# Kernel optimization log

Measured on AMD Instinct MI355X. Metric: run time of the kernel, lower is better.

## Reference

```python
import jax, jax.numpy as jnp
import numpy as np

B, R, A, K, O, I = 50000, 5, 8, 2, 32, 32


def setup_inputs() -> dict:
    key = jax.random.key(0)
    k1, k2, k3 = jax.random.split(key, 3)
    signal = jax.random.normal(k1, (B, R, A, 3, I), dtype=jnp.float32)
    bary = jax.random.uniform(k2, (B, R, A, 3), dtype=jnp.float32)
    # glorot-uniform-ish kernel: shape (R, A, K, O, I)
    limit = np.sqrt(6.0 / (I + O)).astype(np.float32)
    kernel = jax.random.uniform(k3, (R, A, K, O, I), dtype=jnp.float32,
                                minval=-limit, maxval=limit)
    return {"signal": signal, "bary": bary, "kernel": kernel}


def reference(signal, bary, kernel):
    # Barycentric interpolation: pullback[b,r,a,i] = sum_t bary[b,r,a,t] * signal[b,r,a,t,i]
    pullback = jnp.einsum('brat,brati->brai', bary, signal)  # (B,R,A,I)

    n_rot = kernel.shape[1]  # A rotations
    # rotated angular indices: rot_idx[c, a] = (a + c) % A
    rot_idx = (jnp.arange(n_rot)[:, None] + jnp.arange(n_rot)[None, :]) % n_rot
    k_rot = kernel[:, rot_idx]  # (R, C=A, A, K, O, I)

    # conv[b,c,o] = sum_{r,a,k,i} kernel[r,(a+c)%A,k,o,i] * pullback[b,r,a,i]
    conv = jnp.einsum('brai,rcakoi->bco', pullback, k_rot)  # (B, C, O)
    act = jax.nn.relu(conv)

    # Angular max pooling: pick rotation with max euclidean norm over O
    norms = jnp.linalg.norm(act, axis=-1)          # (B, C)
    best = jnp.argmax(norms, axis=-1)              # (B,)
    out = jnp.take_along_axis(act, best[:, None, None], axis=1)[:, 0]  # (B, O)
    return out
```

## Files before the change

kernel.cpp:

```cpp
#include <hip/hip_runtime.h>


#define B_TOT 50000
#define NRA 40

typedef __attribute__((ext_vector_type(8))) short short8v;
typedef __attribute__((ext_vector_type(4))) float f32x4;

__device__ __align__(16) unsigned short W_hi_g[NRA * 256 * 32];
__device__ __align__(16) unsigned short W_lo_g[NRA * 256 * 32];

static __device__ __forceinline__ unsigned short f2bf(float x) {
    unsigned u = __float_as_uint(x);
    u += 0x7FFFu + ((u >> 16) & 1u);
    return (unsigned short)(u >> 16);
}
static __device__ __forceinline__ float bf2f(unsigned short h) {
    return __uint_as_float(((unsigned)h) << 16);
}

static __device__ __forceinline__ void lds_barrier() {
    asm volatile("s_waitcnt lgkmcnt(0)" ::: "memory");
    __builtin_amdgcn_s_barrier();
    asm volatile("" ::: "memory");
}

__global__ __launch_bounds__(256) void build_w_kernel(const float* __restrict__ kern) {
    int e = blockIdx.x * 256 + threadIdx.x;
    int i = e & 31;
    int n = (e >> 5) & 255;
    int ra = e >> 13;
    int r = ra >> 3, a = ra & 7;
    int c = n >> 5, o = n & 31;
    int a2 = (c + a) & 7;
    const float* p = kern + ((((r * 8 + a2) * 2) * 32 + o) * 32 + i);
    float w = p[0] + p[1024];
    unsigned short hi = f2bf(w);
    unsigned short lo = f2bf(w - bf2f(hi));
    W_hi_g[e] = hi;
    W_lo_g[e] = lo;
}

static __device__ __forceinline__ void pcomp(float by0, float by1, float by2,
                                             const float4& a, const float4& b,
                                             const float4& c, float* d) {
    d[0] = fmaf(by2, c.x, fmaf(by1, b.x, by0 * a.x));
    d[1] = fmaf(by2, c.y, fmaf(by1, b.y, by0 * a.y));
    d[2] = fmaf(by2, c.z, fmaf(by1, b.z, by0 * a.z));
    d[3] = fmaf(by2, c.w, fmaf(by1, b.w, by0 * a.w));
}

static __device__ __forceinline__ void pack_write(unsigned short* buf, int idx, const float* v) {
    unsigned short h[4], l[4];
#pragma unroll
    for (int k = 0; k < 4; ++k) {
        h[k] = f2bf(v[k]);
        l[k] = f2bf(v[k] - bf2f(h[k]));
    }
    uint2 H, L;
    H.x = (unsigned)h[0] | ((unsigned)h[1] << 16);
    H.y = (unsigned)h[2] | ((unsigned)h[3] << 16);
    L.x = (unsigned)l[0] | ((unsigned)l[1] << 16);
    L.y = (unsigned)l[2] | ((unsigned)l[3] << 16);
    *(uint2*)(buf + idx) = H;
    *(uint2*)(buf + 2560 + idx) = L;
}

__global__ __launch_bounds__(256, 3) void conv_geo_kernel(const float* __restrict__ sig,
                                                          const float* __restrict__ bary,
                                                          float* __restrict__ out) {
    __shared__ __align__(16) float smem[8448];
    unsigned short* pb0 = (unsigned short*)smem;
    unsigned short* pb1 = pb0 + 5120;

    const int tid  = threadIdx.x;
    const int lane = tid & 63;
    const int wave = tid >> 6;
    const int b_l  = tid >> 2;
    const int q    = tid & 3;
    const int b0   = blockIdx.x * 64;
    int bld = b0 + b_l; if (bld > B_TOT - 1) bld = B_TOT - 1;
    const size_t sig_row = (size_t)bld * 40;

    f32x4 acc[4][4];
#pragma unroll
    for (int mi = 0; mi < 4; ++mi)
#pragma unroll
        for (int ni = 0; ni < 4; ++ni) acc[mi][ni] = (f32x4){0.f, 0.f, 0.f, 0.f};

    const int wcol = (wave * 64 + (lane & 15)) * 32 + (lane >> 4) * 8;
    const int poff = (lane & 15) * 40 + (lane >> 4) * 8;
    const int widx = b_l * 40 + q * 4;

    float4 s0, s1, s2, s3, s4, s5;
    float by0, by1, by2;
    auto load_sig = [&](int ra) {
        const float* sp = sig + (sig_row + ra) * 96 + q * 4;
        s0 = *(const float4*)(sp);      s1 = *(const float4*)(sp + 16);
        s2 = *(const float4*)(sp + 32); s3 = *(const float4*)(sp + 48);
        s4 = *(const float4*)(sp + 64); s5 = *(const float4*)(sp + 80);
        const float* bp = bary + (sig_row + ra) * 3;
        by0 = bp[0]; by1 = bp[1]; by2 = bp[2];
    };
    auto store_p = [&](unsigned short* wrbuf) {
        float pa[4], pbv[4];
        pcomp(by0, by1, by2, s0, s2, s4, pa);
        pcomp(by0, by1, by2, s1, s3, s5, pbv);
        pack_write(wrbuf, widx, pa);
        pack_write(wrbuf, widx + 16, pbv);
    };

    load_sig(0);
    store_p(pb0);
    load_sig(1);
    lds_barrier();

    auto body = [&](int ra, unsigned short* rdbuf, unsigned short* wrbuf) {
        if (ra + 1 < NRA) store_p(wrbuf);
        short8v bh[4], bl[4];
        const unsigned short* whp = W_hi_g + ra * 8192 + wcol;
        const unsigned short* wlp = W_lo_g + ra * 8192 + wcol;
#pragma unroll
        for (int ni = 0; ni < 4; ++ni) {
            bh[ni] = *(const short8v*)(whp + ni * 512);
            bl[ni] = *(const short8v*)(wlp + ni * 512);
        }
        if (ra + 2 < NRA) load_sig(ra + 2);
#pragma unroll
        for (int mi = 0; mi < 4; ++mi) {
            const unsigned short* pr = rdbuf + mi * 640 + poff;
            short8v ah = *(const short8v*)pr;
            short8v al = *(const short8v*)(pr + 2560);
#pragma unroll
            for (int ni = 0; ni < 4; ++ni) {
                acc[mi][ni] = __builtin_amdgcn_mfma_f32_16x16x32_bf16(ah, bh[ni], acc[mi][ni], 0, 0, 0);
                acc[mi][ni] = __builtin_amdgcn_mfma_f32_16x16x32_bf16(ah, bl[ni], acc[mi][ni], 0, 0, 0);
                acc[mi][ni] = __builtin_amdgcn_mfma_f32_16x16x32_bf16(al, bh[ni], acc[mi][ni], 0, 0, 0);
            }
        }
        lds_barrier();
    };

    for (int ra = 0; ra < NRA; ra += 2) {
        body(ra,     pb0, pb1);
        body(ra + 1, pb1, pb0);
    }

    const int colb = wave * 64 + (lane & 15);
    const int rsub = (lane >> 4) * 4;
#pragma unroll
    for (int ph = 0; ph < 2; ++ph) {
        __syncthreads();
#pragma unroll
        for (int mh = 0; mh < 2; ++mh) {
            int mi = ph * 2 + mh;
#pragma unroll
            for (int ni = 0; ni < 4; ++ni)
#pragma unroll
                for (int j = 0; j < 4; ++j)
                    smem[(mh * 16 + rsub + j) * 264 + colb + ni * 16] =
                        fmaxf(acc[mi][ni][j], 0.0f);
        }
        __syncthreads();
        int bb = tid >> 3;
        int c  = tid & 7;
        float n2 = 0.0f;
#pragma unroll
        for (int t = 0; t < 8; ++t) {
            float4 v = *(const float4*)&smem[bb * 264 + c * 32 + t * 4];
            n2 = fmaf(v.x, v.x, n2); n2 = fmaf(v.y, v.y, n2);
            n2 = fmaf(v.z, v.z, n2); n2 = fmaf(v.w, v.w, n2);
        }
        int bc = c;
#pragma unroll
        for (int m = 1; m < 8; m <<= 1) {
            float on2 = __shfl_xor(n2, m, 64);
            int obc = __shfl_xor(bc, m, 64);
            if (on2 > n2 || (on2 == n2 && obc < bc)) { n2 = on2; bc = obc; }
        }
        int b = b0 + ph * 32 + bb;
        if (b < B_TOT) {
            float4 v = *(const float4*)&smem[bb * 264 + bc * 32 + (tid & 7) * 4];
            *(float4*)&out[(size_t)b * 32 + (tid & 7) * 4] = v;
        }
    }
}

extern "C" void kernel_launch(void* const* d_in, const int* in_sizes, int n_in,
                              void* d_out, int out_size, void* d_ws, size_t ws_size,
                              hipStream_t stream) {
    const float* sig  = (const float*)d_in[0];
    const float* bary = (const float*)d_in[1];
    const float* kern = (const float*)d_in[2];
    float* out = (float*)d_out;

    build_w_kernel<<<(NRA * 256 * 32) / 256, 256, 0, stream>>>(kern);
    conv_geo_kernel<<<(B_TOT + 63) / 64, 256, 0, stream>>>(sig, bary, out);
}
```

Before: 231.7 us.

## Deepen signal prefetch to two stages and split W hi/lo loads

Signal and barycentric loads now prefetch two steps ahead using two alternating register sets instead of one step ahead. The W_hi and W_lo fragments are loaded in two phases and share four registers, and the MFMA order is regrouped so independent accumulators are interleaved. The goal is to hide global load latency and lower register pressure from the weight fragments. The extra signal register set adds VGPRs, which could hurt occupancy at 3 waves per SIMD, and the W_lo loads now sit on the critical path in the middle of the body.

```diff
diff --git a/kernel.cpp b/kernel.cpp
--- a/kernel.cpp
+++ b/kernel.cpp
@@ -66,6 +66,11 @@
     *(uint2*)(buf + 2560 + idx) = L;
 }
 
+struct SigSet {
+    float4 s0, s1, s2, s3, s4, s5;
+    float by0, by1, by2;
+};
+
 __global__ __launch_bounds__(256, 3) void conv_geo_kernel(const float* __restrict__ sig,
                                                           const float* __restrict__ bary,
                                                           float* __restrict__ out) {
@@ -92,58 +97,70 @@
     const int poff = (lane & 15) * 40 + (lane >> 4) * 8;
     const int widx = b_l * 40 + q * 4;
 
-    float4 s0, s1, s2, s3, s4, s5;
-    float by0, by1, by2;
-    auto load_sig = [&](int ra) {
+    SigSet SA, SB;
+    auto load_set = [&](SigSet& S, int ra) {
         const float* sp = sig + (sig_row + ra) * 96 + q * 4;
-        s0 = *(const float4*)(sp);      s1 = *(const float4*)(sp + 16);
-        s2 = *(const float4*)(sp + 32); s3 = *(const float4*)(sp + 48);
-        s4 = *(const float4*)(sp + 64); s5 = *(const float4*)(sp + 80);
+        S.s0 = *(const float4*)(sp);      S.s1 = *(const float4*)(sp + 16);
+        S.s2 = *(const float4*)(sp + 32); S.s3 = *(const float4*)(sp + 48);
+        S.s4 = *(const float4*)(sp + 64); S.s5 = *(const float4*)(sp + 80);
         const float* bp = bary + (sig_row + ra) * 3;
-        by0 = bp[0]; by1 = bp[1]; by2 = bp[2];
+        S.by0 = bp[0]; S.by1 = bp[1]; S.by2 = bp[2];
     };
-    auto store_p = [&](unsigned short* wrbuf) {
+    auto store_p = [&](unsigned short* wrbuf, SigSet& S) {
         float pa[4], pbv[4];
-        pcomp(by0, by1, by2, s0, s2, s4, pa);
-        pcomp(by0, by1, by2, s1, s3, s5, pbv);
+        pcomp(S.by0, S.by1, S.by2, S.s0, S.s2, S.s4, pa);
+        pcomp(S.by0, S.by1, S.by2, S.s1, S.s3, S.s5, pbv);
         pack_write(wrbuf, widx, pa);
         pack_write(wrbuf, widx + 16, pbv);
     };
 
-    load_sig(0);
-    store_p(pb0);
-    load_sig(1);
+    load_set(SA, 0);
+    load_set(SB, 1);
+    store_p(pb0, SA);
+    load_set(SA, 2);
     lds_barrier();
 
-    auto body = [&](int ra, unsigned short* rdbuf, unsigned short* wrbuf) {
-        if (ra + 1 < NRA) store_p(wrbuf);
-        short8v bh[4], bl[4];
+    auto body = [&](int ra, unsigned short* rdbuf, unsigned short* wrbuf, SigSet& ready) {
+        if (ra + 1 < NRA) store_p(wrbuf, ready);
+        if (ra + 3 < NRA) load_set(ready, ra + 3);
         const unsigned short* whp = W_hi_g + ra * 8192 + wcol;
         const unsigned short* wlp = W_lo_g + ra * 8192 + wcol;
-#pragma unroll
-        for (int ni = 0; ni < 4; ++ni) {
-            bh[ni] = *(const short8v*)(whp + ni * 512);
-            bl[ni] = *(const short8v*)(wlp + ni * 512);
-        }
-        if (ra + 2 < NRA) load_sig(ra + 2);
+        short8v w0 = *(const short8v*)(whp);
+        short8v w1 = *(const short8v*)(whp + 512);
+        short8v w2 = *(const short8v*)(whp + 1024);
+        short8v w3 = *(const short8v*)(whp + 1536);
 #pragma unroll
         for (int mi = 0; mi < 4; ++mi) {
             const unsigned short* pr = rdbuf + mi * 640 + poff;
             short8v ah = *(const short8v*)pr;
             short8v al = *(const short8v*)(pr + 2560);
-#pragma unroll
-            for (int ni = 0; ni < 4; ++ni) {
-                acc[mi][ni] = __builtin_amdgcn_mfma_f32_16x16x32_bf16(ah, bh[ni], acc[mi][ni], 0, 0, 0);
-                acc[mi][ni] = __builtin_amdgcn_mfma_f32_16x16x32_bf16(ah, bl[ni], acc[mi][ni], 0, 0, 0);
-                acc[mi][ni] = __builtin_amdgcn_mfma_f32_16x16x32_bf16(al, bh[ni], acc[mi][ni], 0, 0, 0);
-            }
+            acc[mi][0] = __builtin_amdgcn_mfma_f32_16x16x32_bf16(ah, w0, acc[mi][0], 0, 0, 0);
+            acc[mi][1] = __builtin_amdgcn_mfma_f32_16x16x32_bf16(ah, w1, acc[mi][1], 0, 0, 0);
+            acc[mi][2] = __builtin_amdgcn_mfma_f32_16x16x32_bf16(ah, w2, acc[mi][2], 0, 0, 0);
+            acc[mi][3] = __builtin_amdgcn_mfma_f32_16x16x32_bf16(ah, w3, acc[mi][3], 0, 0, 0);
+            acc[mi][0] = __builtin_amdgcn_mfma_f32_16x16x32_bf16(al, w0, acc[mi][0], 0, 0, 0);
+            acc[mi][1] = __builtin_amdgcn_mfma_f32_16x16x32_bf16(al, w1, acc[mi][1], 0, 0, 0);
+            acc[mi][2] = __builtin_amdgcn_mfma_f32_16x16x32_bf16(al, w2, acc[mi][2], 0, 0, 0);
+            acc[mi][3] = __builtin_amdgcn_mfma_f32_16x16x32_bf16(al, w3, acc[mi][3], 0, 0, 0);
+        }
+        w0 = *(const short8v*)(wlp);
+        w1 = *(const short8v*)(wlp + 512);
+        w2 = *(const short8v*)(wlp + 1024);
+        w3 = *(const short8v*)(wlp + 1536);
+#pragma unroll
+        for (int mi = 0; mi < 4; ++mi) {
+            short8v ah = *(const short8v*)(rdbuf + mi * 640 + poff);
+            acc[mi][0] = __builtin_amdgcn_mfma_f32_16x16x32_bf16(ah, w0, acc[mi][0], 0, 0, 0);
+            acc[mi][1] = __builtin_amdgcn_mfma_f32_16x16x32_bf16(ah, w1, acc[mi][1], 0, 0, 0);
+            acc[mi][2] = __builtin_amdgcn_mfma_f32_16x16x32_bf16(ah, w2, acc[mi][2], 0, 0, 0);
+            acc[mi][3] = __builtin_amdgcn_mfma_f32_16x16x32_bf16(ah, w3, acc[mi][3], 0, 0, 0);
         }
         lds_barrier();
     };
 
     for (int ra = 0; ra < NRA; ra += 2) {
-        body(ra,     pb0, pb1);
-        body(ra + 1, pb1, pb0);
+        body(ra,     pb0, pb1, SB);
+        body(ra + 1, pb1, pb0, SA);
     }
 
     const int colb = wave * 64 + (lane & 15);
```

Result: slower. 448.2 us (+93.5%).

## Stream raw signal/bary directly into LDS via global_load_lds with double buffering

Applied to the files above, without the earlier changes.

Replaces the per-thread register loads of signal and barycentric weights, followed by interpolation and an LDS store, with asynchronous global_load_lds DMA into a swizzled, double-buffered LDS slot. Each wave then reads its raw operands from LDS, does the barycentric interpolation and bf16 hi/lo split right before the MFMAs, and a manual vmcnt wait plus barrier schedule replaces the old barrier pattern. The aim is to cut VGPR pressure and register staging and to overlap global loads with compute. In exchange, LDS use per block grows and every wave now repeats the interpolation work, since each batch row is computed once per wave.

```diff
diff --git a/kernel.cpp b/kernel.cpp
--- a/kernel.cpp
+++ b/kernel.cpp
@@ -3,9 +3,12 @@
 
 #define B_TOT 50000
 #define NRA 40
+#define SLOT_BYTES 25600
 
 typedef __attribute__((ext_vector_type(8))) short short8v;
 typedef __attribute__((ext_vector_type(4))) float f32x4;
+typedef const __attribute__((address_space(1))) unsigned int* gp1_t;
+typedef __attribute__((address_space(3))) unsigned int* lp3_t;
 
 __device__ __align__(16) unsigned short W_hi_g[NRA * 256 * 32];
 __device__ __align__(16) unsigned short W_lo_g[NRA * 256 * 32];
@@ -17,12 +20,6 @@
 }
 static __device__ __forceinline__ float bf2f(unsigned short h) {
     return __uint_as_float(((unsigned)h) << 16);
-}
-
-static __device__ __forceinline__ void lds_barrier() {
-    asm volatile("s_waitcnt lgkmcnt(0)" ::: "memory");
-    __builtin_amdgcn_s_barrier();
-    asm volatile("" ::: "memory");
 }
 
 __global__ __launch_bounds__(256) void build_w_kernel(const float* __restrict__ kern) {
@@ -41,46 +38,23 @@
     W_lo_g[e] = lo;
 }
 
-static __device__ __forceinline__ void pcomp(float by0, float by1, float by2,
-                                             const float4& a, const float4& b,
-                                             const float4& c, float* d) {
-    d[0] = fmaf(by2, c.x, fmaf(by1, b.x, by0 * a.x));
-    d[1] = fmaf(by2, c.y, fmaf(by1, b.y, by0 * a.y));
-    d[2] = fmaf(by2, c.z, fmaf(by1, b.z, by0 * a.z));
-    d[3] = fmaf(by2, c.w, fmaf(by1, b.w, by0 * a.w));
-}
-
-static __device__ __forceinline__ void pack_write(unsigned short* buf, int idx, const float* v) {
-    unsigned short h[4], l[4];
-#pragma unroll
-    for (int k = 0; k < 4; ++k) {
-        h[k] = f2bf(v[k]);
-        l[k] = f2bf(v[k] - bf2f(h[k]));
-    }
-    uint2 H, L;
-    H.x = (unsigned)h[0] | ((unsigned)h[1] << 16);
-    H.y = (unsigned)h[2] | ((unsigned)h[3] << 16);
-    L.x = (unsigned)l[0] | ((unsigned)l[1] << 16);
-    L.y = (unsigned)l[2] | ((unsigned)l[3] << 16);
-    *(uint2*)(buf + idx) = H;
-    *(uint2*)(buf + 2560 + idx) = L;
+static __device__ __forceinline__ short8v pack8(const unsigned short* h) {
+    union { unsigned u[4]; short8v v; } cv;
+#pragma unroll
+    for (int k = 0; k < 4; ++k)
+        cv.u[k] = (unsigned)h[2 * k] | ((unsigned)h[2 * k + 1] << 16);
+    return cv.v;
 }
 
 __global__ __launch_bounds__(256, 3) void conv_geo_kernel(const float* __restrict__ sig,
                                                           const float* __restrict__ bary,
                                                           float* __restrict__ out) {
-    __shared__ __align__(16) float smem[8448];
-    unsigned short* pb0 = (unsigned short*)smem;
-    unsigned short* pb1 = pb0 + 5120;
+    __shared__ __align__(16) char lds_raw[2 * SLOT_BYTES];
 
     const int tid  = threadIdx.x;
     const int lane = tid & 63;
     const int wave = tid >> 6;
-    const int b_l  = tid >> 2;
-    const int q    = tid & 3;
     const int b0   = blockIdx.x * 64;
-    int bld = b0 + b_l; if (bld > B_TOT - 1) bld = B_TOT - 1;
-    const size_t sig_row = (size_t)bld * 40;
 
     f32x4 acc[4][4];
 #pragma unroll
@@ -89,48 +63,96 @@
         for (int ni = 0; ni < 4; ++ni) acc[mi][ni] = (f32x4){0.f, 0.f, 0.f, 0.f};
 
     const int wcol = (wave * 64 + (lane & 15)) * 32 + (lane >> 4) * 8;
-    const int poff = (lane & 15) * 40 + (lane >> 4) * 8;
-    const int widx = b_l * 40 + q * 4;
-
-    float4 s0, s1, s2, s3, s4, s5;
-    float by0, by1, by2;
-    auto load_sig = [&](int ra) {
-        const float* sp = sig + (sig_row + ra) * 96 + q * 4;
-        s0 = *(const float4*)(sp);      s1 = *(const float4*)(sp + 16);
-        s2 = *(const float4*)(sp + 32); s3 = *(const float4*)(sp + 48);
-        s4 = *(const float4*)(sp + 64); s5 = *(const float4*)(sp + 80);
-        const float* bp = bary + (sig_row + ra) * 3;
-        by0 = bp[0]; by1 = bp[1]; by2 = bp[2];
+
+    unsigned sigoff[6];
+#pragma unroll
+    for (int j = 0; j < 6; ++j) {
+        int L   = j * 4096 + tid * 16;
+        int row = L / 384;
+        int cb  = L - row * 384;
+        int col = cb ^ ((row & 7) << 4);
+        int rowc = b0 + row; if (rowc > B_TOT - 1) rowc = B_TOT - 1;
+        sigoff[j] = (unsigned)rowc * 40u * 384u + (unsigned)col;
+    }
+    unsigned baryoff;
+    {
+        int G  = (tid < 192) ? tid : tid - 192;
+        int rr = G & 63;
+        int t  = G >> 6;
+        int rowc = b0 + rr; if (rowc > B_TOT - 1) rowc = B_TOT - 1;
+        baryoff = (unsigned)rowc * 40u * 12u + (unsigned)t * 4u;
+    }
+
+    const char* sigc  = (const char*)sig;
+    const char* baryc = (const char*)bary;
+    auto issue_slot = [&](int ra, int slot) {
+        char* lb = lds_raw + slot * SLOT_BYTES;
+#pragma unroll
+        for (int j = 0; j < 6; ++j) {
+            const void* gp = sigc + ((size_t)sigoff[j] + (size_t)ra * 384u);
+            void* lp = lb + j * 4096 + tid * 16;
+            __builtin_amdgcn_global_load_lds((gp1_t)gp, (lp3_t)lp, 16, 0, 0);
+        }
+        const void* gpb = baryc + ((size_t)baryoff + (size_t)ra * 12u);
+        void* lpb = lb + 24576 + tid * 4;
+        __builtin_amdgcn_global_load_lds((gp1_t)gpb, (lp3_t)lpb, 4, 0, 0);
     };
-    auto store_p = [&](unsigned short* wrbuf) {
-        float pa[4], pbv[4];
-        pcomp(by0, by1, by2, s0, s2, s4, pa);
-        pcomp(by0, by1, by2, s1, s3, s5, pbv);
-        pack_write(wrbuf, widx, pa);
-        pack_write(wrbuf, widx + 16, pbv);
-    };
-
-    load_sig(0);
-    store_p(pb0);
-    load_sig(1);
-    lds_barrier();
-
-    auto body = [&](int ra, unsigned short* rdbuf, unsigned short* wrbuf) {
-        if (ra + 1 < NRA) store_p(wrbuf);
+
+    issue_slot(0, 0);
+    issue_slot(1, 1);
+
+    const int rr_base = lane & 15;
+    const int i0     = (lane >> 4) * 8;
+
+    for (int ra = 0; ra < NRA; ++ra) {
+        const int slot = ra & 1;
+        if (ra < NRA - 1) asm volatile("s_waitcnt vmcnt(7)" ::: "memory");
+        else              asm volatile("s_waitcnt vmcnt(0)" ::: "memory");
+        __builtin_amdgcn_s_barrier();
+        asm volatile("" ::: "memory");
+
+        const char*  slotc = lds_raw + slot * SLOT_BYTES;
+        const float* bw    = (const float*)(slotc + 24576);
+
         short8v bh[4], bl[4];
-        const unsigned short* whp = W_hi_g + ra * 8192 + wcol;
-        const unsigned short* wlp = W_lo_g + ra * 8192 + wcol;
-#pragma unroll
-        for (int ni = 0; ni < 4; ++ni) {
-            bh[ni] = *(const short8v*)(whp + ni * 512);
-            bl[ni] = *(const short8v*)(wlp + ni * 512);
-        }
-        if (ra + 2 < NRA) load_sig(ra + 2);
+        {
+            const unsigned short* whp = W_hi_g + ra * 8192 + wcol;
+            const unsigned short* wlp = W_lo_g + ra * 8192 + wcol;
+#pragma unroll
+            for (int ni = 0; ni < 4; ++ni) {
+                bh[ni] = *(const short8v*)(whp + ni * 512);
+                bl[ni] = *(const short8v*)(wlp + ni * 512);
+            }
+        }
+
 #pragma unroll
         for (int mi = 0; mi < 4; ++mi) {
-            const unsigned short* pr = rdbuf + mi * 640 + poff;
-            short8v ah = *(const short8v*)pr;
-            short8v al = *(const short8v*)(pr + 2560);
+            const int rr  = mi * 16 + rr_base;
+            const int swz = (rr & 7) << 4;
+            const char* rowp = slotc + rr * 384;
+            float4 a0 = *(const float4*)(rowp + ((  0 + i0 * 4)      ^ swz));
+            float4 a1 = *(const float4*)(rowp + ((  0 + i0 * 4 + 16) ^ swz));
+            float4 b1 = *(const float4*)(rowp + ((128 + i0 * 4)      ^ swz));
+            float4 b2 = *(const float4*)(rowp + ((128 + i0 * 4 + 16) ^ swz));
+            float4 c1 = *(const float4*)(rowp + ((256 + i0 * 4)      ^ swz));
+            float4 c2 = *(const float4*)(rowp + ((256 + i0 * 4 + 16) ^ swz));
+            float by0 = bw[rr], by1 = bw[64 + rr], by2 = bw[128 + rr];
+            float p[8];
+            p[0] = fmaf(by2, c1.x, fmaf(by1, b1.x, by0 * a0.x));
+            p[1] = fmaf(by2, c1.y, fmaf(by1, b1.y, by0 * a0.y));
+            p[2] = fmaf(by2, c1.z, fmaf(by1, b1.z, by0 * a0.z));
+            p[3] = fmaf(by2, c1.w, fmaf(by1, b1.w, by0 * a0.w));
+            p[4] = fmaf(by2, c2.x, fmaf(by1, b2.x, by0 * a1.x));
+            p[5] = fmaf(by2, c2.y, fmaf(by1, b2.y, by0 * a1.y));
+            p[6] = fmaf(by2, c2.z, fmaf(by1, b2.z, by0 * a1.z));
+            p[7] = fmaf(by2, c2.w, fmaf(by1, b2.w, by0 * a1.w));
+            unsigned short hh[8], ll[8];
+#pragma unroll
+            for (int j = 0; j < 8; ++j) {
+                hh[j] = f2bf(p[j]);
+                ll[j] = f2bf(p[j] - bf2f(hh[j]));
+            }
+            short8v ah = pack8(hh), al = pack8(ll);
 #pragma unroll
             for (int ni = 0; ni < 4; ++ni) {
                 acc[mi][ni] = __builtin_amdgcn_mfma_f32_16x16x32_bf16(ah, bh[ni], acc[mi][ni], 0, 0, 0);
@@ -138,14 +160,14 @@
                 acc[mi][ni] = __builtin_amdgcn_mfma_f32_16x16x32_bf16(al, bh[ni], acc[mi][ni], 0, 0, 0);
             }
         }
-        lds_barrier();
-    };
-
-    for (int ra = 0; ra < NRA; ra += 2) {
-        body(ra,     pb0, pb1);
-        body(ra + 1, pb1, pb0);
-    }
-
+
+        asm volatile("" ::: "memory");
+        __builtin_amdgcn_s_barrier();
+        asm volatile("" ::: "memory");
+        if (ra + 2 < NRA) issue_slot(ra + 2, slot);
+    }
+
+    float* smem = (float*)lds_raw;
     const int colb = wave * 64 + (lane & 15);
     const int rsub = (lane >> 4) * 4;
 #pragma unroll
```

New measurement: 289.0 us. 1.25x slower.

## Stream signal tiles into LDS via async global_load_lds with triple-buffered slots

Applied to the files above, without the earlier changes.

Replaces the register-staged signal loads with asynchronous direct global-to-LDS loads into a rotating three-slot buffer, using an XOR swizzle to avoid bank conflicts. Each thread then reads its rows from LDS, computes the barycentric pullback and writes the split bf16 hi/lo operands to a single P buffer before the MFMA loop. The goal is to free registers and hide global memory latency behind compute. The cost is two barriers per iteration instead of one, a larger LDS footprint, and the removal of the occupancy hint from the launch bounds.

```diff
diff --git a/kernel.cpp b/kernel.cpp
--- a/kernel.cpp
+++ b/kernel.cpp
@@ -3,9 +3,13 @@
 
 #define B_TOT 50000
 #define NRA 40
+#define SLOT_B 12288
+#define P_OFF  36864
 
 typedef __attribute__((ext_vector_type(8))) short short8v;
 typedef __attribute__((ext_vector_type(4))) float f32x4;
+typedef const __attribute__((address_space(1))) unsigned int* gp1_t;
+typedef __attribute__((address_space(3))) unsigned int* lp3_t;
 
 __device__ __align__(16) unsigned short W_hi_g[NRA * 256 * 32];
 __device__ __align__(16) unsigned short W_lo_g[NRA * 256 * 32];
@@ -17,12 +21,6 @@
 }
 static __device__ __forceinline__ float bf2f(unsigned short h) {
     return __uint_as_float(((unsigned)h) << 16);
-}
-
-static __device__ __forceinline__ void lds_barrier() {
-    asm volatile("s_waitcnt lgkmcnt(0)" ::: "memory");
-    __builtin_amdgcn_s_barrier();
-    asm volatile("" ::: "memory");
 }
 
 __global__ __launch_bounds__(256) void build_w_kernel(const float* __restrict__ kern) {
@@ -50,28 +48,10 @@
     d[3] = fmaf(by2, c.w, fmaf(by1, b.w, by0 * a.w));
 }
 
-static __device__ __forceinline__ void pack_write(unsigned short* buf, int idx, const float* v) {
-    unsigned short h[4], l[4];
-#pragma unroll
-    for (int k = 0; k < 4; ++k) {
-        h[k] = f2bf(v[k]);
-        l[k] = f2bf(v[k] - bf2f(h[k]));
-    }
-    uint2 H, L;
-    H.x = (unsigned)h[0] | ((unsigned)h[1] << 16);
-    H.y = (unsigned)h[2] | ((unsigned)h[3] << 16);
-    L.x = (unsigned)l[0] | ((unsigned)l[1] << 16);
-    L.y = (unsigned)l[2] | ((unsigned)l[3] << 16);
-    *(uint2*)(buf + idx) = H;
-    *(uint2*)(buf + 2560 + idx) = L;
-}
-
-__global__ __launch_bounds__(256, 3) void conv_geo_kernel(const float* __restrict__ sig,
-                                                          const float* __restrict__ bary,
-                                                          float* __restrict__ out) {
-    __shared__ __align__(16) float smem[8448];
-    unsigned short* pb0 = (unsigned short*)smem;
-    unsigned short* pb1 = pb0 + 5120;
+__global__ __launch_bounds__(256) void conv_geo_kernel(const float* __restrict__ sig,
+                                                       const float* __restrict__ bary,
+                                                       float* __restrict__ out) {
+    __shared__ __align__(16) char lds_raw[45056];
 
     const int tid  = threadIdx.x;
     const int lane = tid & 63;
@@ -80,7 +60,6 @@
     const int q    = tid & 3;
     const int b0   = blockIdx.x * 64;
     int bld = b0 + b_l; if (bld > B_TOT - 1) bld = B_TOT - 1;
-    const size_t sig_row = (size_t)bld * 40;
 
     f32x4 acc[4][4];
 #pragma unroll
@@ -88,49 +67,118 @@
 #pragma unroll
         for (int ni = 0; ni < 4; ++ni) acc[mi][ni] = (f32x4){0.f, 0.f, 0.f, 0.f};
 
-    const int wcol = (wave * 64 + (lane & 15)) * 32 + (lane >> 4) * 8;
-    const int poff = (lane & 15) * 40 + (lane >> 4) * 8;
-    const int widx = b_l * 40 + q * 4;
-
-    float4 s0, s1, s2, s3, s4, s5;
-    float by0, by1, by2;
-    auto load_sig = [&](int ra) {
-        const float* sp = sig + (sig_row + ra) * 96 + q * 4;
-        s0 = *(const float4*)(sp);      s1 = *(const float4*)(sp + 16);
-        s2 = *(const float4*)(sp + 32); s3 = *(const float4*)(sp + 48);
-        s4 = *(const float4*)(sp + 64); s5 = *(const float4*)(sp + 80);
-        const float* bp = bary + (sig_row + ra) * 3;
-        by0 = bp[0]; by1 = bp[1]; by2 = bp[2];
+    const int wcol  = (wave * 64 + (lane & 15)) * 32 + (lane >> 4) * 8;
+    const int pbase = (lane & 15) * 32 + (lane >> 4) * 8;
+    const int widx  = b_l * 32 + q * 4;
+
+    unsigned offA[3], offB[3];
+#pragma unroll
+    for (int j = 0; j < 3; ++j) {
+        int L   = j * 4096 + tid * 16;
+        int rIH = L / 384;
+        int col = L - rIH * 384;
+        int scol = col ^ ((rIH & 7) << 4);
+        int r0 = b0 + rIH;      if (r0 > B_TOT - 1) r0 = B_TOT - 1;
+        int r1 = b0 + 32 + rIH; if (r1 > B_TOT - 1) r1 = B_TOT - 1;
+        offA[j] = (unsigned)r0 * 15360u + (unsigned)scol;
+        offB[j] = (unsigned)r1 * 15360u + (unsigned)scol;
+    }
+    const char* sigc = (const char*)sig;
+    auto issueA = [&](int rra, int slot) {
+#pragma unroll
+        for (int j = 0; j < 3; ++j) {
+            const void* gp = sigc + ((size_t)offA[j] + (size_t)rra * 384u);
+            void* lp = lds_raw + slot * SLOT_B + j * 4096 + tid * 16;
+            __builtin_amdgcn_global_load_lds((gp1_t)gp, (lp3_t)lp, 16, 0, 0);
+        }
     };
-    auto store_p = [&](unsigned short* wrbuf) {
-        float pa[4], pbv[4];
-        pcomp(by0, by1, by2, s0, s2, s4, pa);
-        pcomp(by0, by1, by2, s1, s3, s5, pbv);
-        pack_write(wrbuf, widx, pa);
-        pack_write(wrbuf, widx + 16, pbv);
+    auto issueB = [&](int rra, int slot) {
+#pragma unroll
+        for (int j = 0; j < 3; ++j) {
+            const void* gp = sigc + ((size_t)offB[j] + (size_t)rra * 384u);
+            void* lp = lds_raw + slot * SLOT_B + j * 4096 + tid * 16;
+            __builtin_amdgcn_global_load_lds((gp1_t)gp, (lp3_t)lp, 16, 0, 0);
+        }
     };
 
-    load_sig(0);
-    store_p(pb0);
-    load_sig(1);
-    lds_barrier();
-
-    auto body = [&](int ra, unsigned short* rdbuf, unsigned short* wrbuf) {
-        if (ra + 1 < NRA) store_p(wrbuf);
+    issueA(0, 0);
+    issueB(0, 1);
+    issueA(1, 2);
+
+    int sA = 0, sB = 1;
+    unsigned short* p_w = (unsigned short*)(lds_raw + P_OFF);
+    const unsigned short* p_r = (const unsigned short*)(lds_raw + P_OFF);
+    const int rIHme = b_l & 31;
+    const int hfme  = b_l >> 5;
+    const int swzP  = (b_l & 7) << 4;
+
+#pragma unroll 1
+    for (int ra = 0; ra < NRA; ++ra) {
+        if (ra < NRA - 1) asm volatile("s_waitcnt vmcnt(3) lgkmcnt(0)" ::: "memory");
+        else              asm volatile("s_waitcnt vmcnt(0) lgkmcnt(0)" ::: "memory");
+        __builtin_amdgcn_s_barrier();
+        asm volatile("" ::: "memory");
+
+        const float* bp = bary + (size_t)bld * 120 + ra * 3;
+        float by0 = bp[0], by1 = bp[1], by2 = bp[2];
         short8v bh[4], bl[4];
-        const unsigned short* whp = W_hi_g + ra * 8192 + wcol;
-        const unsigned short* wlp = W_lo_g + ra * 8192 + wcol;
-#pragma unroll
-        for (int ni = 0; ni < 4; ++ni) {
-            bh[ni] = *(const short8v*)(whp + ni * 512);
-            bl[ni] = *(const short8v*)(wlp + ni * 512);
-        }
-        if (ra + 2 < NRA) load_sig(ra + 2);
+        {
+            const unsigned short* wh = W_hi_g + ra * 8192 + wcol;
+            const unsigned short* wl = W_lo_g + ra * 8192 + wcol;
+#pragma unroll
+            for (int ni = 0; ni < 4; ++ni) {
+                bh[ni] = *(const short8v*)(wh + ni * 512);
+                bl[ni] = *(const short8v*)(wl + ni * 512);
+            }
+        }
+
+        {
+            int slotSel = hfme ? sB : sA;
+            const char* rowp = lds_raw + slotSel * SLOT_B + rIHme * 384;
+            float4 s0 = *(const float4*)(rowp + ((q * 16)      ^ swzP));
+            float4 s1 = *(const float4*)(rowp + ((q * 16 + 64) ^ swzP));
+            float4 s2 = *(const float4*)(rowp + (((q * 16)      ^ swzP) + 128));
+            float4 s3 = *(const float4*)(rowp + (((q * 16 + 64) ^ swzP) + 128));
+            float4 s4 = *(const float4*)(rowp + (((q * 16)      ^ swzP) + 256));
+            float4 s5 = *(const float4*)(rowp + (((q * 16 + 64) ^ swzP) + 256));
+            float pa[4], pb2[4];
+            pcomp(by0, by1, by2, s0, s2, s4, pa);
+            pcomp(by0, by1, by2, s1, s3, s5, pb2);
+            unsigned short h1[4], l1[4], h2[4], l2[4];
+#pragma unroll
+            for (int k = 0; k < 4; ++k) {
+                h1[k] = f2bf(pa[k]);  l1[k] = f2bf(pa[k]  - bf2f(h1[k]));
+                h2[k] = f2bf(pb2[k]); l2[k] = f2bf(pb2[k] - bf2f(h2[k]));
+            }
+            uint2 H1, H2, L1, L2;
+            H1.x = (unsigned)h1[0] | ((unsigned)h1[1] << 16);
+            H1.y = (unsigned)h1[2] | ((unsigned)h1[3] << 16);
+            H2.x = (unsigned)h2[0] | ((unsigned)h2[1] << 16);
+            H2.y = (unsigned)h2[2] | ((unsigned)h2[3] << 16);
+            L1.x = (unsigned)l1[0] | ((unsigned)l1[1] << 16);
+            L1.y = (unsigned)l1[2] | ((unsigned)l1[3] << 16);
+            L2.x = (unsigned)l2[0] | ((unsigned)l2[1] << 16);
+            L2.y = (unsigned)l2[2] | ((unsigned)l2[3] << 16);
+            *(uint2*)(p_w + widx)               = H1;
+            *(uint2*)(p_w + widx + 16)          = H2;
+            *(uint2*)(p_w + 2048 + widx)        = L1;
+            *(uint2*)(p_w + 2048 + widx + 16)   = L2;
+        }
+
+        asm volatile("s_waitcnt lgkmcnt(0)" ::: "memory");
+        __builtin_amdgcn_s_barrier();
+        asm volatile("" ::: "memory");
+
+        if (ra + 1 < NRA) issueB(ra + 1, sA);
+        if (ra + 2 < NRA) issueA(ra + 2, sB);
+        sA += 2; if (sA >= 3) sA -= 3;
+        sB += 2; if (sB >= 3) sB -= 3;
+
 #pragma unroll
         for (int mi = 0; mi < 4; ++mi) {
-            const unsigned short* pr = rdbuf + mi * 640 + poff;
+            const unsigned short* pr = p_r + mi * 512 + pbase;
             short8v ah = *(const short8v*)pr;
-            short8v al = *(const short8v*)(pr + 2560);
+            short8v al = *(const short8v*)(pr + 2048);
 #pragma unroll
             for (int ni = 0; ni < 4; ++ni) {
                 acc[mi][ni] = __builtin_amdgcn_mfma_f32_16x16x32_bf16(ah, bh[ni], acc[mi][ni], 0, 0, 0);
@@ -138,14 +186,9 @@
                 acc[mi][ni] = __builtin_amdgcn_mfma_f32_16x16x32_bf16(al, bh[ni], acc[mi][ni], 0, 0, 0);
             }
         }
-        lds_barrier();
-    };
-
-    for (int ra = 0; ra < NRA; ra += 2) {
-        body(ra,     pb0, pb1);
-        body(ra + 1, pb1, pb0);
     }
 
+    float* smem = (float*)lds_raw;
     const int colb = wave * 64 + (lane & 15);
     const int rsub = (lane >> 4) * 4;
 #pragma unroll
```

Measured after the change: 229.1 us. About the same (-1.1%).
